# Kernel optimization log

Measured on AMD Instinct MI355X. Metric: run time of the kernel, lower is better.

Reference implementation:

```python
import jax, jax.numpy as jnp
import numpy as np
from jax import lax

L_MAX = 3          # n_ang_mom: l = 0, 1, 2
M_DIM = 2 * L_MAX - 1  # magnetic components, padded to 5
N_PAIRS = 40000
N_FEAT = 128


def hermite_features(g, n_features):
    """Orthonormal Hermite-function features h_0..h_{F-1}(g); [n] -> [n, F].

    Stable recurrence: h_{k+1} = sqrt(2/(k+1)) g h_k - sqrt(k/(k+1)) h_{k-1}.
    """
    h0 = (np.pi ** -0.25) * jnp.exp(-0.5 * g * g)
    h1 = jnp.sqrt(jnp.asarray(2.0, g.dtype)) * g * h0

    def step(carry, k):
        hkm1, hk = carry
        hkp1 = jnp.sqrt(2.0 / (k + 1.0)) * g * hk - jnp.sqrt(k / (k + 1.0)) * hkm1
        return (hk, hkp1), hkp1

    ks = jnp.arange(1, n_features - 1, dtype=g.dtype)  # produces h_2..h_{F-1}
    _, hs = lax.scan(step, (h0, h1), ks)
    feats = jnp.concatenate([h0[None], h1[None], hs], axis=0)  # [F, n]
    return feats.T  # [n, F]


def tensor_product(cg, a, b):
    """CG-style equivariant contraction.

    cg: [L, M, L, M, L, M] (sparse by selection rules), a, b: [L, M, n, F].
    out[l3, m3, n, f] = sum_{l1 m1 l2 m2} cg[l3,m3,l1,m1,l2,m2] a[l1,m1,n,f] b[l2,m2,n,f]
    """
    return jnp.einsum('lmabpq,abnf,pqnf->lmnf', cg, a, b)


def setup_inputs() -> dict:
    key = jax.random.key(0)
    k0, k1, k2, k3, k4 = jax.random.split(key, 5)
    L, M, N, F = L_MAX, M_DIM, N_PAIRS, N_FEAT
    x = jax.random.normal(k0, (L, M, N, F), dtype=jnp.float32)
    y = jax.random.normal(k1, (L, M, N, F), dtype=jnp.float32)
    g = jax.random.uniform(k2, (N,), dtype=jnp.float32, minval=0.5, maxval=5.0)
    scale = 1.0 / np.sqrt(F)  # GlorotNormal-like scaling
    w1 = jax.random.normal(k3, (F, F), dtype=jnp.float32) * scale
    w2 = jax.random.normal(k4, (F, F), dtype=jnp.float32) * scale
    # Clebsch-Gordan-like coefficient tensor with selection-rule sparsity:
    # nonzero only if |l1-l2| <= l3 <= l1+l2, |m_i| <= l_i, m3 == m1 + m2.
    rng = np.random.default_rng(0)
    cg = np.zeros((L, M, L, M, L, M), dtype=np.float32)
    c = L - 1  # m index offset: m -> m + c
    for l3 in range(L):
        for l1 in range(L):
            for l2 in range(L):
                if not (abs(l1 - l2) <= l3 <= l1 + l2):
                    continue
                for m1 in range(-l1, l1 + 1):
                    for m2 in range(-l2, l2 + 1):
                        m3 = m1 + m2
                        if abs(m3) <= l3:
                            cg[l3, m3 + c, l1, m1 + c, l2, m2 + c] = rng.standard_normal()
    return {"x": x, "y": y, "g": g, "w1": w1, "w2": w2, "cg": jnp.asarray(cg)}


def reference(x, y, g, w1, w2, cg):
    h = hermite_features(g, w1.shape[0])        # [n, F]
    w1g = jnp.einsum('fk,nk->nf', w1, h)        # [n, F]
    w2g = jnp.einsum('fk,nk->nf', w2, h)        # [n, F]
    a1 = w1g[None, None] * x                    # [L, M, n, F]
    b1 = w2g[None, None] * y
    a2 = w1g[None, None] * y
    b2 = w2g[None, None] * x
    res = tensor_product(cg, a1, b1) + tensor_product(cg, a2, b2)
    return res
```

## Files before the change

### kernel.cpp

```cpp
#include <hip/hip_runtime.h>
#include <array>

namespace {

constexpr int NPAIRS = 40000;
constexpr int F = 128;
constexpr long NF = (long)NPAIRS * F;

struct Term {
  int o, a, b;
};

constexpr int count_terms() {
  int idx = 0;
  for (int o = 0; o < 15; ++o) {
    const int l3 = o / 5, m3 = o % 5 - 2;
    if (m3 < -l3 || m3 > l3) continue;
    for (int l1 = 0; l1 < 3; ++l1)
      for (int l2 = 0; l2 < 3; ++l2) {
        const int ld = l1 > l2 ? l1 - l2 : l2 - l1;
        if (l3 < ld || l3 > l1 + l2) continue;
        const int mlo = (-l1 > m3 - l2) ? -l1 : m3 - l2;
        const int mhi = (l1 < m3 + l2) ? l1 : m3 + l2;
        for (int m1 = mlo; m1 <= mhi; ++m1) ++idx;
      }
  }
  return idx;
}
constexpr int NTERMS = count_terms();
static_assert(NTERMS == 117, "term count");

constexpr std::array<Term, NTERMS> make_terms() {
  std::array<Term, NTERMS> t{};
  int idx = 0;
  for (int o = 0; o < 15; ++o) {
    const int l3 = o / 5, m3 = o % 5 - 2;
    if (m3 < -l3 || m3 > l3) continue;
    for (int l1 = 0; l1 < 3; ++l1)
      for (int l2 = 0; l2 < 3; ++l2) {
        const int ld = l1 > l2 ? l1 - l2 : l2 - l1;
        if (l3 < ld || l3 > l1 + l2) continue;
        const int mlo = (-l1 > m3 - l2) ? -l1 : m3 - l2;
        const int mhi = (l1 < m3 + l2) ? l1 : m3 + l2;
        for (int m1 = mlo; m1 <= mhi; ++m1) {
          t[idx].o = o;
          t[idx].a = l1 * 5 + m1 + 2;
          t[idx].b = l2 * 5 + (m3 - m1) + 2;
          ++idx;
        }
      }
  }
  return t;
}
constexpr auto TERMS = make_terms();

constexpr std::array<int, 15> make_acc_idx() {
  std::array<int, 15> m{};
  for (int o = 0; o < 15; ++o) m[o] = -1;
  int q = 0;
  for (int o = 0; o < 15; ++o) {
    const int l3 = o / 5, m3 = o % 5 - 2;
    if (m3 >= -l3 && m3 <= l3) m[o] = q++;
  }
  return m;
}
constexpr auto ACC_IDX = make_acc_idx();

__global__ __launch_bounds__(256, 4) void s_kernel(const float* __restrict__ g,
                                                   const float* __restrict__ w1,
                                                   const float* __restrict__ w2,
                                                   float* __restrict__ s_out) {
  __shared__ float ht[128][32];
  __shared__ float wt1[16][132];
  __shared__ float wt2[16][132];

  const int tid = threadIdx.x;
  const int blk = blockIdx.x;

  if (tid < 32) {
    const float gv = g[blk * 32 + tid];
    float hkm1 = 0.75112554446494248286f * expf(-0.5f * gv * gv);
    float hk = 1.41421356237309504880f * gv * hkm1;
    ht[0][tid] = hkm1;
    ht[1][tid] = hk;
#pragma unroll 1
    for (int k = 1; k <= 126; ++k) {
      const float kf = (float)k;
      const float hkp1 =
          sqrtf(2.0f / (kf + 1.0f)) * gv * hk - sqrtf(kf / (kf + 1.0f)) * hkm1;
      ht[k + 1][tid] = hkp1;
      hkm1 = hk;
      hk = hkp1;
    }
  }

  const int fg = tid & 31;
  const int ng = tid >> 5;

  float acc1[4][4];
  float acc2[4][4];
#pragma unroll
  for (int i = 0; i < 4; ++i)
#pragma unroll
    for (int j = 0; j < 4; ++j) {
      acc1[i][j] = 0.f;
      acc2[i][j] = 0.f;
    }

  for (int kc = 0; kc < 8; ++kc) {
#pragma unroll
    for (int it = 0; it < 2; ++it) {
      const int lin = tid + it * 256;
      const int f = lin >> 2;
      const int kq = lin & 3;
      const float4 v1 = *(const float4*)(w1 + f * 128 + kc * 16 + kq * 4);
      const float4 v2 = *(const float4*)(w2 + f * 128 + kc * 16 + kq * 4);
      wt1[kq * 4 + 0][f] = v1.x;
      wt1[kq * 4 + 1][f] = v1.y;
      wt1[kq * 4 + 2][f] = v1.z;
      wt1[kq * 4 + 3][f] = v1.w;
      wt2[kq * 4 + 0][f] = v2.x;
      wt2[kq * 4 + 1][f] = v2.y;
      wt2[kq * 4 + 2][f] = v2.z;
      wt2[kq * 4 + 3][f] = v2.w;
    }
    __syncthreads();

#pragma unroll
    for (int kk = 0; kk < 16; ++kk) {
      const float4 wv1 = *(const float4*)&wt1[kk][fg * 4];
      const float4 wv2 = *(const float4*)&wt2[kk][fg * 4];
      const float4 ha = *(const float4*)&ht[kc * 16 + kk][ng * 4];
      const float hv[4] = {ha.x, ha.y, ha.z, ha.w};
#pragma unroll
      for (int i = 0; i < 4; ++i) {
        acc1[i][0] = fmaf(hv[i], wv1.x, acc1[i][0]);
        acc1[i][1] = fmaf(hv[i], wv1.y, acc1[i][1]);
        acc1[i][2] = fmaf(hv[i], wv1.z, acc1[i][2]);
        acc1[i][3] = fmaf(hv[i], wv1.w, acc1[i][3]);
        acc2[i][0] = fmaf(hv[i], wv2.x, acc2[i][0]);
        acc2[i][1] = fmaf(hv[i], wv2.y, acc2[i][1]);
        acc2[i][2] = fmaf(hv[i], wv2.z, acc2[i][2]);
        acc2[i][3] = fmaf(hv[i], wv2.w, acc2[i][3]);
      }
    }
    __syncthreads();
  }

#pragma unroll
  for (int i = 0; i < 4; ++i) {
    const long n = (long)blk * 32 + ng * 4 + i;
    float4 sv;
    sv.x = acc1[i][0] * acc2[i][0];
    sv.y = acc1[i][1] * acc2[i][1];
    sv.z = acc1[i][2] * acc2[i][2];
    sv.w = acc1[i][3] * acc2[i][3];
    *(float4*)(s_out + n * 128 + fg * 4) = sv;
  }
}

__global__ __attribute__((amdgpu_waves_per_eu(4, 4)))
__launch_bounds__(256) void tp_kernel(const float* __restrict__ x,
                                      const float* __restrict__ y,
                                      const float* __restrict__ cg,
                                      float* out) {
  __shared__ float d2[NTERMS];
  const int tid = threadIdx.x;
  if (tid < NTERMS) {
    const Term tm = TERMS[tid];
    d2[tid] = cg[(tm.o * 15 + tm.a) * 15 + tm.b] + cg[(tm.o * 15 + tm.b) * 15 + tm.a];
  }
  __syncthreads();

  const long i = (long)blockIdx.x * 256 + tid;
  const long off = 2 * i;

  float2 xv[15], yv[15];
#pragma unroll
  for (int a = 0; a < 15; ++a) xv[a] = *(const float2*)(x + a * NF + off);
#pragma unroll
  for (int b = 0; b < 15; ++b) yv[b] = *(const float2*)(y + b * NF + off);
  const float2 sv = *(const float2*)(out + off);

  float accx[9], accy[9];
#pragma unroll
  for (int q = 0; q < 9; ++q) {
    accx[q] = 0.f;
    accy[q] = 0.f;
  }

#pragma unroll
  for (int t = 0; t < NTERMS; ++t) {
    const int o = TERMS[t].o;
    const int a = TERMS[t].a;
    const int b = TERMS[t].b;
    const int q = ACC_IDX[o];
    const float c = d2[t];
    accx[q] = fmaf(c, xv[a].x * yv[b].x, accx[q]);
    accy[q] = fmaf(c, xv[a].y * yv[b].y, accy[q]);
  }

#pragma unroll
  for (int o = 0; o < 15; ++o) {
    const int q = ACC_IDX[o];
    float2 r;
    if (q >= 0) {
      r.x = accx[q] * sv.x;
      r.y = accy[q] * sv.y;
    } else {
      r.x = 0.f;
      r.y = 0.f;
    }
    *(float2*)(out + o * NF + off) = r;
  }
}

}

extern "C" void kernel_launch(void* const* d_in, const int* in_sizes, int n_in,
                              void* d_out, int out_size, void* d_ws, size_t ws_size,
                              hipStream_t stream) {
  const float* x = (const float*)d_in[0];
  const float* y = (const float*)d_in[1];
  const float* g = (const float*)d_in[2];
  const float* w1 = (const float*)d_in[3];
  const float* w2 = (const float*)d_in[4];
  const float* cg = (const float*)d_in[5];
  float* out = (float*)d_out;

  s_kernel<<<1250, 256, 0, stream>>>(g, w1, w2, out);
  tp_kernel<<<10000, 256, 0, stream>>>(x, y, cg, out);
}
```

Measured before the change: 210.7 us.

## Fuse Hermite projection into tensor-product kernel and skip padded components

Merges the feature-weight kernel into the tensor-product kernel, so each block of four pairs computes the Hermite recurrence and both weight projections in registers. This removes the intermediate write and re-read of the product array. Only the nine valid (l,m) components of x and y are loaded instead of all fifteen, which cuts global reads. In exchange every block reloads the full w1/w2 matrices through shared memory, adding L2 traffic and barriers per block.

```diff
diff --git a/kernel.cpp b/kernel.cpp
--- a/kernel.cpp
+++ b/kernel.cpp
@@ -4,8 +4,7 @@
 namespace {
 
 constexpr int NPAIRS = 40000;
-constexpr int F = 128;
-constexpr long NF = (long)NPAIRS * F;
+constexpr long NF = (long)NPAIRS * 128;
 
 struct Term {
   int o, a, b;
@@ -66,121 +65,115 @@
 }
 constexpr auto ACC_IDX = make_acc_idx();
 
-__global__ __launch_bounds__(256, 4) void s_kernel(const float* __restrict__ g,
-                                                   const float* __restrict__ w1,
-                                                   const float* __restrict__ w2,
-                                                   float* __restrict__ s_out) {
-  __shared__ float ht[128][32];
+constexpr std::array<int, 9> make_used() {
+  std::array<int, 9> u{};
+  int q = 0;
+  for (int o = 0; o < 15; ++o)
+    if (ACC_IDX[o] >= 0) u[q++] = o;
+  return u;
+}
+constexpr auto USED = make_used();
+
+constexpr double csqrt(double x) {
+  double g = x > 1.0 ? x : 1.0;
+  for (int i = 0; i < 64; ++i) g = 0.5 * (g + x / g);
+  return g;
+}
+constexpr std::array<float, 128> make_c1() {
+  std::array<float, 128> a{};
+  for (int k = 0; k < 128; ++k) a[k] = (float)csqrt(2.0 / (k + 1));
+  return a;
+}
+constexpr std::array<float, 128> make_c2() {
+  std::array<float, 128> a{};
+  for (int k = 0; k < 128; ++k) a[k] = (float)csqrt((double)k / (k + 1));
+  return a;
+}
+constexpr auto C1 = make_c1();
+constexpr auto C2 = make_c2();
+
+__global__ __attribute__((amdgpu_waves_per_eu(4, 4)))
+__launch_bounds__(256) void fused_kernel(const float* __restrict__ x,
+                                         const float* __restrict__ y,
+                                         const float* __restrict__ g,
+                                         const float* __restrict__ w1,
+                                         const float* __restrict__ w2,
+                                         const float* __restrict__ cg,
+                                         float* __restrict__ out) {
   __shared__ float wt1[16][132];
   __shared__ float wt2[16][132];
-
-  const int tid = threadIdx.x;
-  const int blk = blockIdx.x;
-
-  if (tid < 32) {
-    const float gv = g[blk * 32 + tid];
-    float hkm1 = 0.75112554446494248286f * expf(-0.5f * gv * gv);
-    float hk = 1.41421356237309504880f * gv * hkm1;
-    ht[0][tid] = hkm1;
-    ht[1][tid] = hk;
-#pragma unroll 1
-    for (int k = 1; k <= 126; ++k) {
-      const float kf = (float)k;
-      const float hkp1 =
-          sqrtf(2.0f / (kf + 1.0f)) * gv * hk - sqrtf(kf / (kf + 1.0f)) * hkm1;
-      ht[k + 1][tid] = hkp1;
-      hkm1 = hk;
-      hk = hkp1;
-    }
-  }
-
-  const int fg = tid & 31;
-  const int ng = tid >> 5;
-
-  float acc1[4][4];
-  float acc2[4][4];
-#pragma unroll
-  for (int i = 0; i < 4; ++i)
-#pragma unroll
-    for (int j = 0; j < 4; ++j) {
-      acc1[i][j] = 0.f;
-      acc2[i][j] = 0.f;
-    }
-
-  for (int kc = 0; kc < 8; ++kc) {
-#pragma unroll
-    for (int it = 0; it < 2; ++it) {
-      const int lin = tid + it * 256;
-      const int f = lin >> 2;
-      const int kq = lin & 3;
-      const float4 v1 = *(const float4*)(w1 + f * 128 + kc * 16 + kq * 4);
-      const float4 v2 = *(const float4*)(w2 + f * 128 + kc * 16 + kq * 4);
-      wt1[kq * 4 + 0][f] = v1.x;
-      wt1[kq * 4 + 1][f] = v1.y;
-      wt1[kq * 4 + 2][f] = v1.z;
-      wt1[kq * 4 + 3][f] = v1.w;
-      wt2[kq * 4 + 0][f] = v2.x;
-      wt2[kq * 4 + 1][f] = v2.y;
-      wt2[kq * 4 + 2][f] = v2.z;
-      wt2[kq * 4 + 3][f] = v2.w;
-    }
-    __syncthreads();
-
-#pragma unroll
-    for (int kk = 0; kk < 16; ++kk) {
-      const float4 wv1 = *(const float4*)&wt1[kk][fg * 4];
-      const float4 wv2 = *(const float4*)&wt2[kk][fg * 4];
-      const float4 ha = *(const float4*)&ht[kc * 16 + kk][ng * 4];
-      const float hv[4] = {ha.x, ha.y, ha.z, ha.w};
-#pragma unroll
-      for (int i = 0; i < 4; ++i) {
-        acc1[i][0] = fmaf(hv[i], wv1.x, acc1[i][0]);
-        acc1[i][1] = fmaf(hv[i], wv1.y, acc1[i][1]);
-        acc1[i][2] = fmaf(hv[i], wv1.z, acc1[i][2]);
-        acc1[i][3] = fmaf(hv[i], wv1.w, acc1[i][3]);
-        acc2[i][0] = fmaf(hv[i], wv2.x, acc2[i][0]);
-        acc2[i][1] = fmaf(hv[i], wv2.y, acc2[i][1]);
-        acc2[i][2] = fmaf(hv[i], wv2.z, acc2[i][2]);
-        acc2[i][3] = fmaf(hv[i], wv2.w, acc2[i][3]);
-      }
-    }
-    __syncthreads();
-  }
-
-#pragma unroll
-  for (int i = 0; i < 4; ++i) {
-    const long n = (long)blk * 32 + ng * 4 + i;
-    float4 sv;
-    sv.x = acc1[i][0] * acc2[i][0];
-    sv.y = acc1[i][1] * acc2[i][1];
-    sv.z = acc1[i][2] * acc2[i][2];
-    sv.w = acc1[i][3] * acc2[i][3];
-    *(float4*)(s_out + n * 128 + fg * 4) = sv;
-  }
-}
-
-__global__ __attribute__((amdgpu_waves_per_eu(4, 4)))
-__launch_bounds__(256) void tp_kernel(const float* __restrict__ x,
-                                      const float* __restrict__ y,
-                                      const float* __restrict__ cg,
-                                      float* out) {
-  __shared__ float d2[NTERMS];
+  __shared__ float d2s[NTERMS];
+
   const int tid = threadIdx.x;
   if (tid < NTERMS) {
     const Term tm = TERMS[tid];
-    d2[tid] = cg[(tm.o * 15 + tm.a) * 15 + tm.b] + cg[(tm.o * 15 + tm.b) * 15 + tm.a];
-  }
-  __syncthreads();
-
-  const long i = (long)blockIdx.x * 256 + tid;
-  const long off = 2 * i;
-
-  float2 xv[15], yv[15];
-#pragma unroll
-  for (int a = 0; a < 15; ++a) xv[a] = *(const float2*)(x + a * NF + off);
-#pragma unroll
-  for (int b = 0; b < 15; ++b) yv[b] = *(const float2*)(y + b * NF + off);
-  const float2 sv = *(const float2*)(out + off);
+    d2s[tid] = cg[(tm.o * 15 + tm.a) * 15 + tm.b] + cg[(tm.o * 15 + tm.b) * 15 + tm.a];
+  }
+
+  const int u = tid & 63;
+  const int nl = tid >> 6;
+  const long n = (long)blockIdx.x * 4 + nl;
+  const long off = n * 128 + 2 * u;
+
+  float2 xv[9], yv[9];
+#pragma unroll
+  for (int q = 0; q < 9; ++q) xv[q] = *(const float2*)(x + (long)USED[q] * NF + off);
+#pragma unroll
+  for (int q = 0; q < 9; ++q) yv[q] = *(const float2*)(y + (long)USED[q] * NF + off);
+
+  const float gv = g[n];
+  float hprev = 0.f;
+  float hcur = 0.75112554446494248286f * expf(-0.5f * gv * gv);
+  float2 dot1 = make_float2(0.f, 0.f);
+  float2 dot2 = make_float2(0.f, 0.f);
+
+  const int fr = tid >> 1;
+  const int half = tid & 1;
+
+#pragma unroll
+  for (int kc = 0; kc < 8; ++kc) {
+    const float* wp1 = w1 + fr * 128 + kc * 16 + half * 8;
+    const float* wp2 = w2 + fr * 128 + kc * 16 + half * 8;
+    const float4 a0 = *(const float4*)(wp1);
+    const float4 a1 = *(const float4*)(wp1 + 4);
+    const float4 b0 = *(const float4*)(wp2);
+    const float4 b1 = *(const float4*)(wp2 + 4);
+    __syncthreads();
+    const int k0 = half * 8;
+    wt1[k0 + 0][fr] = a0.x;
+    wt1[k0 + 1][fr] = a0.y;
+    wt1[k0 + 2][fr] = a0.z;
+    wt1[k0 + 3][fr] = a0.w;
+    wt1[k0 + 4][fr] = a1.x;
+    wt1[k0 + 5][fr] = a1.y;
+    wt1[k0 + 6][fr] = a1.z;
+    wt1[k0 + 7][fr] = a1.w;
+    wt2[k0 + 0][fr] = b0.x;
+    wt2[k0 + 1][fr] = b0.y;
+    wt2[k0 + 2][fr] = b0.z;
+    wt2[k0 + 3][fr] = b0.w;
+    wt2[k0 + 4][fr] = b1.x;
+    wt2[k0 + 5][fr] = b1.y;
+    wt2[k0 + 6][fr] = b1.z;
+    wt2[k0 + 7][fr] = b1.w;
+    __syncthreads();
+
+#pragma unroll
+    for (int kk = 0; kk < 16; ++kk) {
+      const int k = kc * 16 + kk;
+      const float2 wa = *(const float2*)&wt1[kk][2 * u];
+      const float2 wb = *(const float2*)&wt2[kk][2 * u];
+      dot1.x = fmaf(wa.x, hcur, dot1.x);
+      dot1.y = fmaf(wa.y, hcur, dot1.y);
+      dot2.x = fmaf(wb.x, hcur, dot2.x);
+      dot2.y = fmaf(wb.y, hcur, dot2.y);
+      const float hnext = C1[k] * gv * hcur - C2[k] * hprev;
+      hprev = hcur;
+      hcur = hnext;
+    }
+  }
+
+  const float2 sv = make_float2(dot1.x * dot2.x, dot1.y * dot2.y);
 
   float accx[9], accy[9];
 #pragma unroll
@@ -191,13 +184,12 @@
 
 #pragma unroll
   for (int t = 0; t < NTERMS; ++t) {
-    const int o = TERMS[t].o;
-    const int a = TERMS[t].a;
-    const int b = TERMS[t].b;
-    const int q = ACC_IDX[o];
-    const float c = d2[t];
-    accx[q] = fmaf(c, xv[a].x * yv[b].x, accx[q]);
-    accy[q] = fmaf(c, xv[a].y * yv[b].y, accy[q]);
+    const int qo = ACC_IDX[TERMS[t].o];
+    const int qa = ACC_IDX[TERMS[t].a];
+    const int qb = ACC_IDX[TERMS[t].b];
+    const float c = d2s[t];
+    accx[qo] = fmaf(c, xv[qa].x * yv[qb].x, accx[qo]);
+    accy[qo] = fmaf(c, xv[qa].y * yv[qb].y, accy[qo]);
   }
 
 #pragma unroll
@@ -211,7 +203,7 @@
       r.x = 0.f;
       r.y = 0.f;
     }
-    *(float2*)(out + o * NF + off) = r;
+    *(float2*)(out + (long)o * NF + off) = r;
   }
 }
 
@@ -228,6 +220,5 @@
   const float* cg = (const float*)d_in[5];
   float* out = (float*)d_out;
 
-  s_kernel<<<1250, 256, 0, stream>>>(g, w1, w2, out);
-  tp_kernel<<<10000, 256, 0, stream>>>(x, y, cg, out);
-}
+  fused_kernel<<<10000, 256, 0, stream>>>(x, y, g, w1, w2, cg, out);
+}
```

New measurement: 376.9 us. 1.79x slower.
